# Kernel optimization log

Measured on AMD Instinct MI355X. Metric: run time of the kernel, lower is better.

## Reference

```python
import jax, jax.numpy as jnp
import numpy as np

B, S, D, E, K = 4, 4096, 2048, 64, 2

def setup_inputs() -> dict:
    key = jax.random.key(0)
    kx, kw = jax.random.split(key)
    x = jax.random.normal(kx, (B, S, D), dtype=jnp.float32)
    W = jax.random.normal(kw, (E, D), dtype=jnp.float32) * (1.0 / np.sqrt(D))
    b = jnp.zeros((E,), dtype=jnp.float32)
    return {"x": x, "W": W, "b": b, "k": K}

def reference(x, W, b, k):
    # logits: [B, S, E]
    logits = jnp.einsum('bsd,ed->bse', x, W) + b
    probs = jax.nn.softmax(logits, axis=-1)
    topk_probs, topk_experts = jax.lax.top_k(probs, k)  # [B,S,k]
    # one-hot over experts, OR-reduce over k -> bool mask [B,S,E]
    onehot = jax.nn.one_hot(topk_experts, E, dtype=jnp.int32)  # [B,S,k,E]
    masks = onehot.sum(axis=-2).astype(jnp.bool_)
    return (masks, probs)
```

## Files before the change

### kernel.cpp

```cpp
#include <hip/hip_runtime.h>
#include <math.h>

#define NTOK    16384
#define DDIM    2048
#define NEXP    64
#define PSTRIDE (NTOK * NEXP)
#define KP      128
#define NPH     16
#define PLANE_H 8192
#define SLICE_B 32768

#define AS1 __attribute__((address_space(1)))
#define AS3 __attribute__((address_space(3)))

typedef _Float16 half8   __attribute__((ext_vector_type(8)));
typedef float    floatx4 __attribute__((ext_vector_type(4)));

__global__ __launch_bounds__(256) void wconv_kernel(
    const float* __restrict__ W, _Float16* __restrict__ ws)
{
    const int g     = blockIdx.x * 256 + threadIdx.x;
    const int p     = g >> 11;
    const int L     = g & 2047;
    const int plane = L >> 10;
    const int e     = (L >> 4) & 63;
    const int cp    = L & 15;
    const int c     = cp ^ (e & 7);
    const int k     = (p << 7) + (c << 3);

    const float* src = &W[(size_t)e * DDIM + k];
    floatx4 w0 = *(const floatx4*)src;
    floatx4 w1 = *(const floatx4*)(src + 4);

    half8 o;
#pragma unroll
    for (int i = 0; i < 4; ++i) {
        float f0 = w0[i], f1 = w1[i];
        _Float16 h0 = (_Float16)f0, h1 = (_Float16)f1;
        if (plane == 0) { o[i] = h0; o[4 + i] = h1; }
        else {
            o[i]     = (_Float16)((f0 - (float)h0) * 2048.0f);
            o[4 + i] = (_Float16)((f1 - (float)h1) * 2048.0f);
        }
    }
    *(half8*)((char*)ws + (size_t)g * 16) = o;
}

__global__ __launch_bounds__(256, 2) void router_kernel(
    const float* __restrict__ x,
    const _Float16* __restrict__ ws,
    const float* __restrict__ bias,
    float* __restrict__ out)
{
    __shared__ _Float16 lds[2][SLICE_B / 2];

    const int tid  = threadIdx.x;
    const int lane = tid & 63;
    const int wid  = tid >> 6;
    const int t    = wid >> 1;
    const int h    = wid & 1;
    const int t0   = blockIdx.x * 32 + t * 16;
    const int mrow = lane & 15;
    const int quad = lane >> 4;

    floatx4 acc_hh[4], acc_md[4];
#pragma unroll
    for (int j = 0; j < 4; ++j) { acc_hh[j] = (floatx4)0.0f; acc_md[j] = (floatx4)0.0f; }

    const float* xrow = x + (size_t)(t0 + mrow) * DDIM + h * 64 + quad * 8;

    const char* gslice0 = (const char*)ws;
    char*       lbase[2] = { (char*)&lds[0][0] + wid * 8192,
                             (char*)&lds[1][0] + wid * 8192 };

#define STAGE(P, BUF)                                                          \
    {                                                                          \
        const char* gsrc = gslice0 + (size_t)(P) * SLICE_B + wid * 8192 + lane * 16; \
        char*       ldst = lbase[BUF];                                         \
        _Pragma("unroll")                                                      \
        for (int i = 0; i < 8; ++i)                                            \
            __builtin_amdgcn_global_load_lds(                                  \
                (const AS1 unsigned int*)(const void*)(gsrc + i * 1024),       \
                (AS3 unsigned int*)(void*)(ldst + i * 1024), 16, 0, 0);        \
    }

    floatx4 xc[4], xn[4];

    STAGE(0, 0);
#pragma unroll
    for (int s = 0; s < 2; ++s) {
        xc[2 * s]     = *(const floatx4*)(xrow + s * 32);
        xc[2 * s + 1] = *(const floatx4*)(xrow + s * 32 + 4);
    }
    __syncthreads();

#pragma unroll 2
    for (int p = 0; p < NPH; ++p) {
        if (p < NPH - 1) {
            STAGE(p + 1, (p + 1) & 1);
            const float* xp = xrow + (p + 1) * KP;
#pragma unroll
            for (int s = 0; s < 2; ++s) {
                xn[2 * s]     = *(const floatx4*)(xp + s * 32);
                xn[2 * s + 1] = *(const floatx4*)(xp + s * 32 + 4);
            }
        }

        const _Float16* lb = &lds[p & 1][0];
#pragma unroll
        for (int s = 0; s < 2; ++s) {
            half8 a_hi, a_lo;
#pragma unroll
            for (int i = 0; i < 4; ++i) {
                float fv = xc[2 * s][i];
                _Float16 hh = (_Float16)fv;
                a_hi[i] = hh;
                a_lo[i] = (_Float16)((fv - (float)hh) * 2048.0f);
            }
#pragma unroll
            for (int i = 0; i < 4; ++i) {
                float fv = xc[2 * s + 1][i];
                _Float16 hh = (_Float16)fv;
                a_hi[4 + i] = hh;
                a_lo[4 + i] = (_Float16)((fv - (float)hh) * 2048.0f);
            }
#pragma unroll
            for (int j = 0; j < 4; ++j) {
                const int e   = j * 16 + mrow;
                const int c   = h * 8 + s * 4 + quad;
                const int off = e * 128 + ((c ^ (e & 7)) << 3);
                half8 bh = *(const half8*)(lb + off);
                half8 bl = *(const half8*)(lb + PLANE_H + off);
                acc_hh[j] = __builtin_amdgcn_mfma_f32_16x16x32_f16(a_hi, bh, acc_hh[j], 0, 0, 0);
                acc_md[j] = __builtin_amdgcn_mfma_f32_16x16x32_f16(a_hi, bl, acc_md[j], 0, 0, 0);
                acc_md[j] = __builtin_amdgcn_mfma_f32_16x16x32_f16(a_lo, bh, acc_md[j], 0, 0, 0);
            }
        }

        if (p < NPH - 1) {
#pragma unroll
            for (int i = 0; i < 4; ++i) xc[i] = xn[i];
        }
        __syncthreads();
    }

    float lg[4][4];
#pragma unroll
    for (int j = 0; j < 4; ++j)
#pragma unroll
        for (int r = 0; r < 4; ++r)
            lg[j][r] = acc_hh[j][r] + acc_md[j][r] * (1.0f / 2048.0f);

    float* rbuf = (float*)&lds[0][0];
    if (h == 1) {
#pragma unroll
        for (int j = 0; j < 4; ++j)
#pragma unroll
            for (int r = 0; r < 4; ++r)
                rbuf[t * 1024 + (j * 4 + r) * 64 + lane] = lg[j][r];
    }
    __syncthreads();
    if (h == 1) return;

#pragma unroll
    for (int j = 0; j < 4; ++j) {
        const float bj = bias[j * 16 + mrow];
#pragma unroll
        for (int r = 0; r < 4; ++r)
            lg[j][r] += rbuf[t * 1024 + (j * 4 + r) * 64 + lane] + bj;
    }

    const int c = mrow;
#pragma unroll
    for (int r = 0; r < 4; ++r) {
        const int trow = t0 + quad * 4 + r;

        float m = lg[0][r];
#pragma unroll
        for (int j = 1; j < 4; ++j) m = fmaxf(m, lg[j][r]);
#pragma unroll
        for (int off = 1; off <= 8; off <<= 1) m = fmaxf(m, __shfl_xor(m, off));

        float pj[4], s = 0.0f;
#pragma unroll
        for (int j = 0; j < 4; ++j) { pj[j] = __expf(lg[j][r] - m); s += pj[j]; }
#pragma unroll
        for (int off = 1; off <= 8; off <<= 1) s += __shfl_xor(s, off);
        const float rinv = 1.0f / s;

        float v1 = -1e30f, v2 = -1e30f; int i1 = -1, i2 = -1;
#pragma unroll
        for (int j = 0; j < 4; ++j) {
            float v = lg[j][r]; int e = j * 16 + c;
            if (v > v1 || (v == v1 && e < i1)) { v2 = v1; i2 = i1; v1 = v; i1 = e; }
            else if (v > v2 || (v == v2 && e < i2)) { v2 = v; i2 = e; }
        }
#pragma unroll
        for (int off = 1; off <= 8; off <<= 1) {
            float u1 = __shfl_xor(v1, off); int q1 = __shfl_xor(i1, off);
            float u2 = __shfl_xor(v2, off); int q2 = __shfl_xor(i2, off);
            if (u1 > v1 || (u1 == v1 && q1 < i1)) {
                if (v1 > u2 || (v1 == u2 && i1 < q2)) { v2 = v1; i2 = i1; }
                else                                   { v2 = u2; i2 = q2; }
                v1 = u1; i1 = q1;
            } else {
                if (u1 > v2 || (u1 == v2 && q1 < i2)) { v2 = u1; i2 = q1; }
            }
        }

#pragma unroll
        for (int j = 0; j < 4; ++j) {
            const int col = j * 16 + c;
            const size_t o = (size_t)trow * NEXP + col;
            out[o]           = (col == i1 || col == i2) ? 1.0f : 0.0f;
            out[PSTRIDE + o] = pj[j] * rinv;
        }
    }
}

extern "C" void kernel_launch(void* const* d_in, const int* in_sizes, int n_in,
                              void* d_out, int out_size, void* d_ws, size_t ws_size,
                              hipStream_t stream) {
    const float* x = (const float*)d_in[0];
    const float* W = (const float*)d_in[1];
    const float* b = (const float*)d_in[2];
    (void)in_sizes; (void)n_in; (void)out_size; (void)ws_size;
    float* out = (float*)d_out;

    _Float16* ws = (_Float16*)d_ws;

    hipLaunchKernelGGL(wconv_kernel, dim3(128), dim3(256), 0, stream, W, ws);
    hipLaunchKernelGGL(router_kernel, dim3(NTOK / 32), dim3(256), 0, stream, x, ws, b, out);
}
```

Before: 201.7 us.

## Load weight fragments directly from global into registers, dropping LDS staging

The weight conversion kernel now writes plain row-major hi and lo fp16 planes instead of a swizzled per-phase slice layout. The router kernel no longer stages weight slices into double-buffered LDS with per-phase barriers. Each wave instead loads its B fragments straight from global memory (relying on L1/L2 caching) into register double buffers, in a software-pipelined loop that is unrolled by four. This removes the LDS round-trip and the __syncthreads in the main loop, at the cost of more redundant global/L1 weight traffic per block and higher register pressure. The last pipeline iterations issue a few wrapped-around prefetch loads that are never used.

Result: slower. 245.4 us (+21.7%).

```diff
diff --git a/kernel.cpp b/kernel.cpp
--- a/kernel.cpp
+++ b/kernel.cpp
@@ -5,13 +5,7 @@
 #define DDIM    2048
 #define NEXP    64
 #define PSTRIDE (NTOK * NEXP)
-#define KP      128
-#define NPH     16
-#define PLANE_H 8192
-#define SLICE_B 32768
-
-#define AS1 __attribute__((address_space(1)))
-#define AS3 __attribute__((address_space(3)))
+#define WHALF   (NEXP * DDIM)
 
 typedef _Float16 half8   __attribute__((ext_vector_type(8)));
 typedef float    floatx4 __attribute__((ext_vector_type(4)));
@@ -19,31 +13,26 @@
 __global__ __launch_bounds__(256) void wconv_kernel(
     const float* __restrict__ W, _Float16* __restrict__ ws)
 {
-    const int g     = blockIdx.x * 256 + threadIdx.x;
-    const int p     = g >> 11;
-    const int L     = g & 2047;
-    const int plane = L >> 10;
-    const int e     = (L >> 4) & 63;
-    const int cp    = L & 15;
-    const int c     = cp ^ (e & 7);
-    const int k     = (p << 7) + (c << 3);
-
-    const float* src = &W[(size_t)e * DDIM + k];
+    const int g   = blockIdx.x * 256 + threadIdx.x;
+    const int e   = g >> 8;
+    const int pos = (g & 255) * 8;
+
+    const float* src = &W[(size_t)e * DDIM + pos];
     floatx4 w0 = *(const floatx4*)src;
     floatx4 w1 = *(const floatx4*)(src + 4);
 
-    half8 o;
+    half8 hi, lo;
 #pragma unroll
     for (int i = 0; i < 4; ++i) {
         float f0 = w0[i], f1 = w1[i];
         _Float16 h0 = (_Float16)f0, h1 = (_Float16)f1;
-        if (plane == 0) { o[i] = h0; o[4 + i] = h1; }
-        else {
-            o[i]     = (_Float16)((f0 - (float)h0) * 2048.0f);
-            o[4 + i] = (_Float16)((f1 - (float)h1) * 2048.0f);
-        }
-    }
-    *(half8*)((char*)ws + (size_t)g * 16) = o;
+        hi[i]     = h0; lo[i]     = (_Float16)((f0 - (float)h0) * 2048.0f);
+        hi[4 + i] = h1; lo[4 + i] = (_Float16)((f1 - (float)h1) * 2048.0f);
+    }
+
+    _Float16* dst = ws + (size_t)e * DDIM + pos;
+    *(half8*)dst           = hi;
+    *(half8*)(dst + WHALF) = lo;
 }
 
 __global__ __launch_bounds__(256, 2) void router_kernel(
@@ -52,7 +41,7 @@
     const float* __restrict__ bias,
     float* __restrict__ out)
 {
-    __shared__ _Float16 lds[2][SLICE_B / 2];
+    __shared__ float rbuf[2048];
 
     const int tid  = threadIdx.x;
     const int lane = tid & 63;
@@ -67,81 +56,73 @@
 #pragma unroll
     for (int j = 0; j < 4; ++j) { acc_hh[j] = (floatx4)0.0f; acc_md[j] = (floatx4)0.0f; }
 
-    const float* xrow = x + (size_t)(t0 + mrow) * DDIM + h * 64 + quad * 8;
-
-    const char* gslice0 = (const char*)ws;
-    char*       lbase[2] = { (char*)&lds[0][0] + wid * 8192,
-                             (char*)&lds[1][0] + wid * 8192 };
-
-#define STAGE(P, BUF)                                                          \
-    {                                                                          \
-        const char* gsrc = gslice0 + (size_t)(P) * SLICE_B + wid * 8192 + lane * 16; \
-        char*       ldst = lbase[BUF];                                         \
-        _Pragma("unroll")                                                      \
-        for (int i = 0; i < 8; ++i)                                            \
-            __builtin_amdgcn_global_load_lds(                                  \
-                (const AS1 unsigned int*)(const void*)(gsrc + i * 1024),       \
-                (AS3 unsigned int*)(void*)(ldst + i * 1024), 16, 0, 0);        \
-    }
-
-    floatx4 xc[4], xn[4];
-
-    STAGE(0, 0);
-#pragma unroll
-    for (int s = 0; s < 2; ++s) {
-        xc[2 * s]     = *(const floatx4*)(xrow + s * 32);
-        xc[2 * s + 1] = *(const floatx4*)(xrow + s * 32 + 4);
-    }
-    __syncthreads();
-
-#pragma unroll 2
-    for (int p = 0; p < NPH; ++p) {
-        if (p < NPH - 1) {
-            STAGE(p + 1, (p + 1) & 1);
-            const float* xp = xrow + (p + 1) * KP;
-#pragma unroll
-            for (int s = 0; s < 2; ++s) {
-                xn[2 * s]     = *(const floatx4*)(xp + s * 32);
-                xn[2 * s + 1] = *(const floatx4*)(xp + s * 32 + 4);
-            }
-        }
-
-        const _Float16* lb = &lds[p & 1][0];
-#pragma unroll
-        for (int s = 0; s < 2; ++s) {
-            half8 a_hi, a_lo;
-#pragma unroll
-            for (int i = 0; i < 4; ++i) {
-                float fv = xc[2 * s][i];
-                _Float16 hh = (_Float16)fv;
-                a_hi[i] = hh;
-                a_lo[i] = (_Float16)((fv - (float)hh) * 2048.0f);
-            }
-#pragma unroll
-            for (int i = 0; i < 4; ++i) {
-                float fv = xc[2 * s + 1][i];
-                _Float16 hh = (_Float16)fv;
-                a_hi[4 + i] = hh;
-                a_lo[4 + i] = (_Float16)((fv - (float)hh) * 2048.0f);
-            }
-#pragma unroll
-            for (int j = 0; j < 4; ++j) {
-                const int e   = j * 16 + mrow;
-                const int c   = h * 8 + s * 4 + quad;
-                const int off = e * 128 + ((c ^ (e & 7)) << 3);
-                half8 bh = *(const half8*)(lb + off);
-                half8 bl = *(const half8*)(lb + PLANE_H + off);
-                acc_hh[j] = __builtin_amdgcn_mfma_f32_16x16x32_f16(a_hi, bh, acc_hh[j], 0, 0, 0);
-                acc_md[j] = __builtin_amdgcn_mfma_f32_16x16x32_f16(a_hi, bl, acc_md[j], 0, 0, 0);
-                acc_md[j] = __builtin_amdgcn_mfma_f32_16x16x32_f16(a_lo, bh, acc_md[j], 0, 0, 0);
-            }
-        }
-
-        if (p < NPH - 1) {
-#pragma unroll
-            for (int i = 0; i < 4; ++i) xc[i] = xn[i];
-        }
-        __syncthreads();
+#define KOF(v) (((((v) >> 1) * 128) + (((v) & 1) * 32)) & (DDIM - 1))
+
+    const float*    xrow = x  + (size_t)(t0 + mrow) * DDIM + h * 64 + quad * 8;
+    const _Float16* whi  = ws + (size_t)mrow * DDIM        + h * 64 + quad * 8;
+    const _Float16* wlo  = whi + WHALF;
+
+#define LOADB(BH, BL, KOFF)                                                   \
+    {                                                                         \
+        const int _ko = (KOFF);                                               \
+        _Pragma("unroll")                                                     \
+        for (int j = 0; j < 4; ++j) {                                         \
+            BH[j] = *(const half8*)(whi + j * (16 * DDIM) + _ko);             \
+            BL[j] = *(const half8*)(wlo + j * (16 * DDIM) + _ko);             \
+        }                                                                     \
+    }
+
+#define LOADX(X0, X1, KOFF)                                                   \
+    {                                                                         \
+        const int _ko = (KOFF);                                               \
+        X0 = *(const floatx4*)(xrow + _ko);                                   \
+        X1 = *(const floatx4*)(xrow + _ko + 4);                               \
+    }
+
+#define COMPUTE(X0, X1, BH, BL)                                               \
+    {                                                                         \
+        half8 a_hi, a_lo;                                                     \
+        _Pragma("unroll")                                                     \
+        for (int i = 0; i < 4; ++i) {                                         \
+            float f0 = (X0)[i], f1 = (X1)[i];                                 \
+            _Float16 h0 = (_Float16)f0, h1 = (_Float16)f1;                    \
+            a_hi[i]     = h0; a_lo[i]     = (_Float16)((f0 - (float)h0) * 2048.0f); \
+            a_hi[4 + i] = h1; a_lo[4 + i] = (_Float16)((f1 - (float)h1) * 2048.0f); \
+        }                                                                     \
+        _Pragma("unroll")                                                     \
+        for (int j = 0; j < 4; ++j) {                                         \
+            acc_hh[j] = __builtin_amdgcn_mfma_f32_16x16x32_f16(a_hi, (BH)[j], acc_hh[j], 0, 0, 0); \
+            acc_md[j] = __builtin_amdgcn_mfma_f32_16x16x32_f16(a_hi, (BL)[j], acc_md[j], 0, 0, 0); \
+            acc_md[j] = __builtin_amdgcn_mfma_f32_16x16x32_f16(a_lo, (BH)[j], acc_md[j], 0, 0, 0); \
+        }                                                                     \
+    }
+
+    half8   bh0[4], bl0[4], bh1[4], bl1[4];
+    floatx4 X0a, X0b, X1a, X1b, X2a, X2b, X3a, X3b;
+
+    LOADX(X0a, X0b, KOF(0))
+    LOADX(X1a, X1b, KOF(1))
+    LOADX(X2a, X2b, KOF(2))
+    LOADB(bh0, bl0, KOF(0))
+    LOADB(bh1, bl1, KOF(1))
+
+#pragma unroll 1
+    for (int u = 0; u < 32; u += 4) {
+        LOADX(X3a, X3b, KOF(u + 3))
+        COMPUTE(X0a, X0b, bh0, bl0)
+        LOADB(bh0, bl0, KOF(u + 2))
+
+        LOADX(X0a, X0b, KOF(u + 4))
+        COMPUTE(X1a, X1b, bh1, bl1)
+        LOADB(bh1, bl1, KOF(u + 3))
+
+        LOADX(X1a, X1b, KOF(u + 5))
+        COMPUTE(X2a, X2b, bh0, bl0)
+        LOADB(bh0, bl0, KOF(u + 4))
+
+        LOADX(X2a, X2b, KOF(u + 6))
+        COMPUTE(X3a, X3b, bh1, bl1)
+        LOADB(bh1, bl1, KOF(u + 5))
     }
 
     float lg[4][4];
@@ -151,7 +132,6 @@
         for (int r = 0; r < 4; ++r)
             lg[j][r] = acc_hh[j][r] + acc_md[j][r] * (1.0f / 2048.0f);
 
-    float* rbuf = (float*)&lds[0][0];
     if (h == 1) {
 #pragma unroll
         for (int j = 0; j < 4; ++j)
@@ -229,6 +209,6 @@
 
     _Float16* ws = (_Float16*)d_ws;
 
-    hipLaunchKernelGGL(wconv_kernel, dim3(128), dim3(256), 0, stream, W, ws);
+    hipLaunchKernelGGL(wconv_kernel, dim3(64), dim3(256), 0, stream, W, ws);
     hipLaunchKernelGGL(router_kernel, dim3(NTOK / 32), dim3(256), 0, stream, x, ws, b, out);
 }
```

## Triple-buffer W and x slices through LDS with async global_load_lds

Applied to the files above, without the earlier changes.

The K loop becomes 32 phases of 64 elements, and both the fp16 W split planes and the fp32 x tile are staged into LDS with global_load_lds into a three-deep ring buffer. Explicit vmcnt waits and barriers replace __syncthreads, so loads run two phases ahead of compute. This is meant to hide global load latency better and to drop the register-prefetched x loads. In exchange there are twice as many barriers, more LDS per block, and hand-counted waitcnt values that must match the number of issued loads exactly.

Measured after the change: 209.8 us. 1.04x slower.

```diff
diff --git a/kernel.cpp b/kernel.cpp
--- a/kernel.cpp
+++ b/kernel.cpp
@@ -5,10 +5,10 @@
 #define DDIM    2048
 #define NEXP    64
 #define PSTRIDE (NTOK * NEXP)
-#define KP      128
-#define NPH     16
-#define PLANE_H 8192
-#define SLICE_B 32768
+#define NPH     32
+#define WSLICE  16384
+#define XSLICE  8192
+#define NBUF    3
 
 #define AS1 __attribute__((address_space(1)))
 #define AS3 __attribute__((address_space(3)))
@@ -20,13 +20,13 @@
     const float* __restrict__ W, _Float16* __restrict__ ws)
 {
     const int g     = blockIdx.x * 256 + threadIdx.x;
-    const int p     = g >> 11;
-    const int L     = g & 2047;
-    const int plane = L >> 10;
-    const int e     = (L >> 4) & 63;
-    const int cp    = L & 15;
+    const int p     = g >> 10;
+    const int L     = g & 1023;
+    const int plane = L >> 9;
+    const int e     = (L >> 3) & 63;
+    const int cp    = L & 7;
     const int c     = cp ^ (e & 7);
-    const int k     = (p << 7) + (c << 3);
+    const int k     = (p << 6) + (c << 3);
 
     const float* src = &W[(size_t)e * DDIM + k];
     floatx4 w0 = *(const floatx4*)src;
@@ -52,14 +52,16 @@
     const float* __restrict__ bias,
     float* __restrict__ out)
 {
-    __shared__ _Float16 lds[2][SLICE_B / 2];
+    __shared__ _Float16 lw[NBUF * 8192];
+    __shared__ float    lx[NBUF * 2048];
 
     const int tid  = threadIdx.x;
     const int lane = tid & 63;
     const int wid  = tid >> 6;
     const int t    = wid >> 1;
     const int h    = wid & 1;
-    const int t0   = blockIdx.x * 32 + t * 16;
+    const int t0b  = blockIdx.x * 32;
+    const int t0   = t0b + t * 16;
     const int mrow = lane & 15;
     const int quad = lane >> 4;
 
@@ -67,82 +69,91 @@
 #pragma unroll
     for (int j = 0; j < 4; ++j) { acc_hh[j] = (floatx4)0.0f; acc_md[j] = (floatx4)0.0f; }
 
-    const float* xrow = x + (size_t)(t0 + mrow) * DDIM + h * 64 + quad * 8;
-
-    const char* gslice0 = (const char*)ws;
-    char*       lbase[2] = { (char*)&lds[0][0] + wid * 8192,
-                             (char*)&lds[1][0] + wid * 8192 };
+    const char* gw = (const char*)ws + wid * 4096 + lane * 16;
+    const int L0 = wid * 128 + lane;
+    const int L1 = L0 + 64;
+    const int r0 = L0 >> 4, c0g = (L0 & 15) ^ (r0 & 15);
+    const int r1 = L1 >> 4, c1g = (L1 & 15) ^ (r1 & 15);
+    const char* gx0 = (const char*)(x + (size_t)(t0b + r0) * DDIM + c0g * 4);
+    const char* gx1 = (const char*)(x + (size_t)(t0b + r1) * DDIM + c1g * 4);
 
 #define STAGE(P, BUF)                                                          \
     {                                                                          \
-        const char* gsrc = gslice0 + (size_t)(P) * SLICE_B + wid * 8192 + lane * 16; \
-        char*       ldst = lbase[BUF];                                         \
+        const char* gsw = gw + (size_t)(P) * WSLICE;                           \
+        char*       ldw = (char*)lw + (BUF) * WSLICE + wid * 4096;             \
         _Pragma("unroll")                                                      \
-        for (int i = 0; i < 8; ++i)                                            \
+        for (int i = 0; i < 4; ++i)                                            \
             __builtin_amdgcn_global_load_lds(                                  \
-                (const AS1 unsigned int*)(const void*)(gsrc + i * 1024),       \
-                (AS3 unsigned int*)(void*)(ldst + i * 1024), 16, 0, 0);        \
-    }
-
-    floatx4 xc[4], xn[4];
-
-    STAGE(0, 0);
-#pragma unroll
-    for (int s = 0; s < 2; ++s) {
-        xc[2 * s]     = *(const floatx4*)(xrow + s * 32);
-        xc[2 * s + 1] = *(const floatx4*)(xrow + s * 32 + 4);
-    }
-    __syncthreads();
-
-#pragma unroll 2
-    for (int p = 0; p < NPH; ++p) {
-        if (p < NPH - 1) {
-            STAGE(p + 1, (p + 1) & 1);
-            const float* xp = xrow + (p + 1) * KP;
-#pragma unroll
-            for (int s = 0; s < 2; ++s) {
-                xn[2 * s]     = *(const floatx4*)(xp + s * 32);
-                xn[2 * s + 1] = *(const floatx4*)(xp + s * 32 + 4);
-            }
-        }
-
-        const _Float16* lb = &lds[p & 1][0];
-#pragma unroll
-        for (int s = 0; s < 2; ++s) {
-            half8 a_hi, a_lo;
-#pragma unroll
-            for (int i = 0; i < 4; ++i) {
-                float fv = xc[2 * s][i];
-                _Float16 hh = (_Float16)fv;
-                a_hi[i] = hh;
-                a_lo[i] = (_Float16)((fv - (float)hh) * 2048.0f);
-            }
-#pragma unroll
-            for (int i = 0; i < 4; ++i) {
-                float fv = xc[2 * s + 1][i];
-                _Float16 hh = (_Float16)fv;
-                a_hi[4 + i] = hh;
-                a_lo[4 + i] = (_Float16)((fv - (float)hh) * 2048.0f);
-            }
-#pragma unroll
-            for (int j = 0; j < 4; ++j) {
-                const int e   = j * 16 + mrow;
-                const int c   = h * 8 + s * 4 + quad;
-                const int off = e * 128 + ((c ^ (e & 7)) << 3);
-                half8 bh = *(const half8*)(lb + off);
-                half8 bl = *(const half8*)(lb + PLANE_H + off);
-                acc_hh[j] = __builtin_amdgcn_mfma_f32_16x16x32_f16(a_hi, bh, acc_hh[j], 0, 0, 0);
-                acc_md[j] = __builtin_amdgcn_mfma_f32_16x16x32_f16(a_hi, bl, acc_md[j], 0, 0, 0);
-                acc_md[j] = __builtin_amdgcn_mfma_f32_16x16x32_f16(a_lo, bh, acc_md[j], 0, 0, 0);
-            }
-        }
-
-        if (p < NPH - 1) {
-#pragma unroll
-            for (int i = 0; i < 4; ++i) xc[i] = xn[i];
-        }
-        __syncthreads();
-    }
+                (const AS1 unsigned int*)(const void*)(gsw + i * 1024),        \
+                (AS3 unsigned int*)(void*)(ldw + i * 1024), 16, 0, 0);         \
+        char* ldx = (char*)lx + (BUF) * XSLICE + wid * 2048;                   \
+        __builtin_amdgcn_global_load_lds(                                      \
+            (const AS1 unsigned int*)(const void*)(gx0 + (size_t)(P) * 256),   \
+            (AS3 unsigned int*)(void*)(ldx), 16, 0, 0);                        \
+        __builtin_amdgcn_global_load_lds(                                      \
+            (const AS1 unsigned int*)(const void*)(gx1 + (size_t)(P) * 256),   \
+            (AS3 unsigned int*)(void*)(ldx + 1024), 16, 0, 0);                 \
+    }
+
+#define COMPUTE(BUF)                                                           \
+    {                                                                          \
+        const _Float16* wb = lw + (BUF) * 8192;                                \
+        const float*    xb = lx + (BUF) * 2048;                                \
+        const int xrow = t * 16 + mrow;                                        \
+        const int cc0  = h * 8 + quad * 2;                                     \
+        floatx4 X0 = *(const floatx4*)(xb + xrow * 64 + ((cc0 ^ mrow) << 2));  \
+        floatx4 X1 = *(const floatx4*)(xb + xrow * 64 + (((cc0 + 1) ^ mrow) << 2)); \
+        half8 a_hi, a_lo;                                                      \
+        _Pragma("unroll")                                                      \
+        for (int i = 0; i < 4; ++i) {                                          \
+            float f0 = X0[i], f1 = X1[i];                                      \
+            _Float16 h0 = (_Float16)f0, h1 = (_Float16)f1;                     \
+            a_hi[i]     = h0; a_lo[i]     = (_Float16)((f0 - (float)h0) * 2048.0f); \
+            a_hi[4 + i] = h1; a_lo[4 + i] = (_Float16)((f1 - (float)h1) * 2048.0f); \
+        }                                                                      \
+        _Pragma("unroll")                                                      \
+        for (int j = 0; j < 4; ++j) {                                          \
+            const int e   = j * 16 + mrow;                                     \
+            const int c   = h * 4 + quad;                                      \
+            const int off = e * 64 + ((c ^ (e & 7)) << 3);                     \
+            half8 bh = *(const half8*)(wb + off);                              \
+            half8 bl = *(const half8*)(wb + 4096 + off);                       \
+            acc_hh[j] = __builtin_amdgcn_mfma_f32_16x16x32_f16(a_hi, bh, acc_hh[j], 0, 0, 0); \
+            acc_md[j] = __builtin_amdgcn_mfma_f32_16x16x32_f16(a_hi, bl, acc_md[j], 0, 0, 0); \
+            acc_md[j] = __builtin_amdgcn_mfma_f32_16x16x32_f16(a_lo, bh, acc_md[j], 0, 0, 0); \
+        }                                                                      \
+    }
+
+#define PHASE(P, BUF, BUF2)                                                    \
+    {                                                                          \
+        __builtin_amdgcn_s_barrier();                                          \
+        asm volatile("" ::: "memory");                                         \
+        STAGE(P + 2, BUF2)                                                     \
+        asm volatile("s_waitcnt vmcnt(12)" ::: "memory");                      \
+        __builtin_amdgcn_s_barrier();                                          \
+        asm volatile("" ::: "memory");                                         \
+        COMPUTE(BUF)                                                           \
+    }
+
+    STAGE(0, 0)
+    STAGE(1, 1)
+
+#pragma unroll 1
+    for (int p3 = 0; p3 < NPH - 2; p3 += 3) {
+        PHASE(p3 + 0, 0, 2)
+        PHASE(p3 + 1, 1, 0)
+        PHASE(p3 + 2, 2, 1)
+    }
+    __builtin_amdgcn_s_barrier();
+    asm volatile("" ::: "memory");
+    asm volatile("s_waitcnt vmcnt(6)" ::: "memory");
+    __builtin_amdgcn_s_barrier();
+    asm volatile("" ::: "memory");
+    COMPUTE(0)
+    asm volatile("s_waitcnt vmcnt(0)" ::: "memory");
+    __builtin_amdgcn_s_barrier();
+    asm volatile("" ::: "memory");
+    COMPUTE(1)
 
     float lg[4][4];
 #pragma unroll
@@ -151,7 +162,7 @@
         for (int r = 0; r < 4; ++r)
             lg[j][r] = acc_hh[j][r] + acc_md[j][r] * (1.0f / 2048.0f);
 
-    float* rbuf = (float*)&lds[0][0];
+    float* rbuf = (float*)lw;
     if (h == 1) {
 #pragma unroll
         for (int j = 0; j < 4; ++j)
```
